# Kernel tuning notes

Measured on AMD Instinct MI355X. Metric: run time of the kernel, lower is better.

Reference implementation:

```python
import jax, jax.numpy as jnp
import numpy as np

D = 2048  # d_model
B = 64    # batch
S = 32    # seq_len (module is designed for 32-step sequences)
C = 8     # number of control embeddings
INITRANGE = 0.1


def setup_inputs() -> dict:
    key = jax.random.key(0)
    ks = jax.random.split(key, 6)

    def lin_w(k):
        return jax.random.uniform(k, (D, D), minval=-INITRANGE, maxval=INITRANGE, dtype=jnp.float32)

    zb = jnp.zeros((D,), dtype=jnp.float32)
    return {
        "sequence": jax.random.normal(ks[0], (B, S, D), dtype=jnp.float32),
        "controls": jax.random.normal(ks[1], (C, B, D), dtype=jnp.float32),
        "Wq": lin_w(ks[2]), "bq": zb,
        "Wk": lin_w(ks[3]), "bk": zb,
        "Wv": lin_w(ks[4]), "bv": zb,
        "Wo": lin_w(ks[5]), "bo": zb,
    }


def reference(sequence, controls, Wq, bq, Wk, bk, Wv, bv, Wo, bo):
    # sequence: (B, S, D); controls: (C, B, D) = stacked list of control embeddings.
    d = sequence.shape[-1]
    queries = sequence @ Wq.T + bq            # (B, S, D)
    keys = controls @ Wk.T + bk               # (C, B, D)  == control_key(c).unsqueeze(1)
    values = controls @ Wv.T + bv             # (C, B, D)
    # bmm(queries, keys^T) with a single key per control -> scores (C, B, S, 1)
    scores = jnp.einsum('bsd,cbd->cbs', queries, keys)[..., None] / jnp.sqrt(jnp.asarray(d, sequence.dtype))
    attn = jax.nn.softmax(scores, axis=-1)    # softmax over a size-1 axis -> exactly 1.0
    attended = attn * values[:, :, None, :]   # (C, B, S, D); bmm(attn, values)
    # dropout is identity in eval mode
    projected = jnp.einsum('cbsd,ed->cbse', attended, Wo) + bo  # per-control output_proj
    # residual accumulation over the control loop == sum over C
    return sequence + projected.sum(axis=0)
```

## Files before the change

kernel.cpp:

```cpp
#include <hip/hip_runtime.h>
#include <hip/hip_bf16.h>

#define DM 2048
#define BB 64
#define SS 32
#define CC 8

typedef __attribute__((ext_vector_type(8))) short short8;
typedef __attribute__((ext_vector_type(4))) short short4v;
typedef __attribute__((ext_vector_type(4))) float f32x4;

static __device__ __forceinline__ short f2bf(float f) {
  union { __hip_bfloat16 h; short s; } u;
  u.h = __float2bfloat16(f);
  return u.s;
}

__global__ void k1_sum_bf16(const float* __restrict__ controls,
                            short* __restrict__ u16) {
  const int idx = blockIdx.x * 128 + threadIdx.x;
  const int b = idx >> 9;
  const int k = (idx & 511) * 4;
  float4 s = make_float4(0.f, 0.f, 0.f, 0.f);
#pragma unroll
  for (int c = 0; c < CC; ++c) {
    const float4 v = *reinterpret_cast<const float4*>(
        controls + ((size_t)c * BB + b) * DM + k);
    s.x += v.x; s.y += v.y; s.z += v.z; s.w += v.w;
  }
  short4v o = {f2bf(s.x), f2bf(s.y), f2bf(s.z), f2bf(s.w)};
  *reinterpret_cast<short4v*>(u16 + (size_t)b * DM + k) = o;
}

__global__ __launch_bounds__(256, 2) void gemm_v16(
    const short* __restrict__ abf, const float* __restrict__ w,
    const float* __restrict__ bias, short* __restrict__ vout) {
  __shared__ float lwW[4][2][16 * 128];
  __shared__ f32x4 red[3][64];

  const int t    = threadIdx.x;
  const int lane = t & 63;
  const int wv   = t >> 6;
  const int e0   = (blockIdx.x & 127) * 16;
  const int b0   = (blockIdx.x >> 7) * 16;
  const int kq   = wv * 512;

  const int wrl = lane >> 5, wg = lane & 31;
  const int r = lane & 15, ksub = lane >> 4;
  const int q = r & 7;

  const short* abase = abf + (size_t)(b0 + r) * DM + kq + ksub * 8;
  short8 areg[2][4];
  f32x4 acc = {0.f, 0.f, 0.f, 0.f};

#define ISSUE_W(c, bsel)                                                      \
  {                                                                           \
    const int ck = kq + (c) * 128;                                            \
    float* wd = &lwW[wv][bsel][0];                                            \
    _Pragma("unroll") for (int i = 0; i < 8; ++i) {                           \
      const int row = 2 * i + wrl;                                            \
      const float* src =                                                      \
          w + (size_t)(e0 + row) * DM + ck + ((wg ^ (row & 7)) << 2);         \
      __builtin_amdgcn_global_load_lds(                                       \
          (const __attribute__((address_space(1))) void*)src,                 \
          (__attribute__((address_space(3))) void*)(wd + i * 256), 16, 0, 0); \
    }                                                                         \
  }
#define LOAD_A(c, bsel)                                                       \
  {                                                                           \
    _Pragma("unroll") for (int s = 0; s < 4; ++s) areg[bsel][s] =             \
        *reinterpret_cast<const short8*>(abase + (c) * 128 + s * 32);         \
  }

  ISSUE_W(0, 0)
  LOAD_A(0, 0)

#pragma unroll
  for (int c = 0; c < 4; ++c) {
    if (c < 3) {
      ISSUE_W(c + 1, (c + 1) & 1)
      LOAD_A(c + 1, (c + 1) & 1)
      asm volatile("s_waitcnt vmcnt(12)" ::: "memory");
    } else {
      asm volatile("s_waitcnt vmcnt(0)" ::: "memory");
    }
    __builtin_amdgcn_sched_barrier(0);

    const float* wb = &lwW[wv][c & 1][0];
#pragma unroll
    for (int s = 0; s < 4; ++s) {
      const int gl = s * 8 + ksub * 2;
      const float4 lo =
          *reinterpret_cast<const float4*>(wb + r * 128 + ((gl ^ q) << 2));
      const float4 hi = *reinterpret_cast<const float4*>(
          wb + r * 128 + (((gl + 1) ^ q) << 2));
      short8 bf;
      bf[0] = f2bf(lo.x); bf[1] = f2bf(lo.y);
      bf[2] = f2bf(lo.z); bf[3] = f2bf(lo.w);
      bf[4] = f2bf(hi.x); bf[5] = f2bf(hi.y);
      bf[6] = f2bf(hi.z); bf[7] = f2bf(hi.w);
      acc = __builtin_amdgcn_mfma_f32_16x16x32_bf16(areg[c & 1][s], bf, acc,
                                                    0, 0, 0);
    }
  }
#undef ISSUE_W
#undef LOAD_A

  if (wv != 0) red[wv - 1][lane] = acc;
  __syncthreads();
  if (wv == 0) {
#pragma unroll
    for (int i = 0; i < 3; ++i) acc += red[i][lane];
    const float be = 8.f * bias[e0 + r];
#pragma unroll
    for (int j = 0; j < 4; ++j)
      vout[(size_t)(b0 + ksub * 4 + j) * DM + e0 + r] = f2bf(acc[j] + be);
  }
}

__global__ __launch_bounds__(512, 2) void gemm_out(
    const short* __restrict__ abf, const float* __restrict__ w,
    const float* __restrict__ bias, const float* __restrict__ seq,
    float* __restrict__ out) {
  __shared__ float lwW[8][2][16 * 64];
  __shared__ f32x4 red[2][3][64];
  __shared__ float ptt[16][32];

  const int t    = threadIdx.x;
  const int lane = t & 63;
  const int wv   = t >> 6;
  const int eh   = wv & 1;
  const int kqi  = wv >> 1;
  const int e0   = (blockIdx.x & 63) * 32;
  const int b0   = (blockIdx.x >> 6) * 16;
  const int ew   = e0 + eh * 16;
  const int kq   = kqi * 512;

  const int rl4 = lane >> 4, g = lane & 15;
  const int r = lane & 15, ksub = lane >> 4;

  const short* abase = abf + (size_t)(b0 + r) * DM + kq + ksub * 8;
  short8 areg[2][2];
  f32x4 acc = {0.f, 0.f, 0.f, 0.f};

  const int bl = t >> 5, rem = t & 31;
  const int ef4 = (rem & 7) * 4, sl = rem >> 3;
  float4 sreg[8];

#define ISSUE_W2(c, bsel)                                                     \
  {                                                                           \
    const int ck = kq + (c) * 64;                                             \
    float* wd = &lwW[wv][bsel][0];                                            \
    _Pragma("unroll") for (int i = 0; i < 4; ++i) {                           \
      const int row = 4 * i + rl4;                                            \
      const float* src =                                                      \
          w + (size_t)(ew + row) * DM + ck + ((g ^ row) << 2);                \
      __builtin_amdgcn_global_load_lds(                                       \
          (const __attribute__((address_space(1))) void*)src,                 \
          (__attribute__((address_space(3))) void*)(wd + i * 256), 16, 0, 0); \
    }                                                                         \
  }
#define LOAD_A2(c, bsel)                                                      \
  {                                                                           \
    areg[bsel][0] = *reinterpret_cast<const short8*>(abase + (c) * 64);       \
    areg[bsel][1] = *reinterpret_cast<const short8*>(abase + (c) * 64 + 32);  \
  }

  ISSUE_W2(0, 0)
  LOAD_A2(0, 0)

#pragma unroll
  for (int c = 0; c < 8; ++c) {
    if (c < 7) {
      ISSUE_W2(c + 1, (c + 1) & 1)
      LOAD_A2(c + 1, (c + 1) & 1)
      asm volatile("s_waitcnt vmcnt(6)" ::: "memory");
    } else {
#pragma unroll
      for (int i = 0; i < 8; ++i) {
        const size_t off =
            ((size_t)(b0 + bl) * SS + (sl + 4 * i)) * DM + e0 + ef4;
        sreg[i] = *reinterpret_cast<const float4*>(seq + off);
      }
      asm volatile("s_waitcnt vmcnt(8)" ::: "memory");
    }
    __builtin_amdgcn_sched_barrier(0);

    const float* wb = &lwW[wv][c & 1][0];
#pragma unroll
    for (int s = 0; s < 2; ++s) {
      const int gl = s * 8 + ksub * 2;
      const float4 lo =
          *reinterpret_cast<const float4*>(wb + r * 64 + ((gl ^ r) << 2));
      const float4 hi = *reinterpret_cast<const float4*>(
          wb + r * 64 + (((gl + 1) ^ r) << 2));
      short8 bf;
      bf[0] = f2bf(lo.x); bf[1] = f2bf(lo.y);
      bf[2] = f2bf(lo.z); bf[3] = f2bf(lo.w);
      bf[4] = f2bf(hi.x); bf[5] = f2bf(hi.y);
      bf[6] = f2bf(hi.z); bf[7] = f2bf(hi.w);
      acc = __builtin_amdgcn_mfma_f32_16x16x32_bf16(areg[c & 1][s], bf, acc,
                                                    0, 0, 0);
    }
  }
#undef ISSUE_W2
#undef LOAD_A2

  if (kqi != 0) red[eh][kqi - 1][lane] = acc;
  __syncthreads();
  if (kqi == 0) {
#pragma unroll
    for (int i = 0; i < 3; ++i) acc += red[eh][i][lane];
    const float be = 8.f * bias[ew + r];
#pragma unroll
    for (int j = 0; j < 4; ++j) ptt[ksub * 4 + j][eh * 16 + r] = acc[j] + be;
  }
  __syncthreads();

  const float4 pv = *reinterpret_cast<const float4*>(&ptt[bl][ef4]);
  asm volatile("s_waitcnt vmcnt(0)" ::: "memory");
#pragma unroll
  for (int i = 0; i < 8; ++i) {
    const size_t off = ((size_t)(b0 + bl) * SS + (sl + 4 * i)) * DM + e0 + ef4;
    *reinterpret_cast<float4*>(out + off) =
        make_float4(sreg[i].x + pv.x, sreg[i].y + pv.y, sreg[i].z + pv.z,
                    sreg[i].w + pv.w);
  }
}

extern "C" void kernel_launch(void* const* d_in, const int* in_sizes, int n_in,
                              void* d_out, int out_size, void* d_ws,
                              size_t ws_size, hipStream_t stream) {
  const float* seq      = (const float*)d_in[0];
  const float* controls = (const float*)d_in[1];
  const float* Wv = (const float*)d_in[6];
  const float* bv = (const float*)d_in[7];
  const float* Wo = (const float*)d_in[8];
  const float* bo = (const float*)d_in[9];
  float* out = (float*)d_out;

  char* ws = (char*)d_ws;
  short* u16 = (short*)(ws);
  short* v16 = (short*)(ws + (512ull << 10));

  k1_sum_bf16<<<256, 128, 0, stream>>>(controls, u16);
  gemm_v16<<<512, 256, 0, stream>>>(u16, Wv, bv, v16);
  gemm_out<<<256, 512, 0, stream>>>(v16, Wo, bo, seq, out);
}
```

Before: 30.49 us.

## Fuse control-sum kernel into first GEMM via grid-wide atomic barrier

Folds the control-embedding sum/bf16 conversion into the first GEMM kernel. Each block computes a slice of the summed controls, then all blocks wait on a global atomic counter before starting the GEMM. This removes one kernel launch but adds a memset launch and a spin barrier that assumes all 512 blocks are co-resident. Separately, the output GEMM now interleaves the sequence residual loads across the k-loop instead of issuing them all at the end.

```diff
diff --git a/kernel.cpp b/kernel.cpp
--- a/kernel.cpp
+++ b/kernel.cpp
@@ -5,6 +5,7 @@
 #define BB 64
 #define SS 32
 #define CC 8
+#define NBA 512
 
 typedef __attribute__((ext_vector_type(8))) short short8;
 typedef __attribute__((ext_vector_type(4))) short short4v;
@@ -16,40 +17,52 @@
   return u.s;
 }
 
-__global__ void k1_sum_bf16(const float* __restrict__ controls,
-                            short* __restrict__ u16) {
-  const int idx = blockIdx.x * 128 + threadIdx.x;
-  const int b = idx >> 9;
-  const int k = (idx & 511) * 4;
-  float4 s = make_float4(0.f, 0.f, 0.f, 0.f);
-#pragma unroll
-  for (int c = 0; c < CC; ++c) {
-    const float4 v = *reinterpret_cast<const float4*>(
-        controls + ((size_t)c * BB + b) * DM + k);
-    s.x += v.x; s.y += v.y; s.z += v.z; s.w += v.w;
-  }
-  short4v o = {f2bf(s.x), f2bf(s.y), f2bf(s.z), f2bf(s.w)};
-  *reinterpret_cast<short4v*>(u16 + (size_t)b * DM + k) = o;
-}
-
-__global__ __launch_bounds__(256, 2) void gemm_v16(
-    const short* __restrict__ abf, const float* __restrict__ w,
-    const float* __restrict__ bias, short* __restrict__ vout) {
+__global__ __launch_bounds__(256, 2) void fused_u_gemm1(
+    const float* __restrict__ controls, const float* __restrict__ w,
+    const float* __restrict__ bias, short* __restrict__ u16,
+    short* __restrict__ vout, int* __restrict__ bar) {
   __shared__ float lwW[4][2][16 * 128];
   __shared__ f32x4 red[3][64];
 
-  const int t    = threadIdx.x;
+  const int t   = threadIdx.x;
+  const int bid = blockIdx.x;
+
+  if (t < 64) {
+    const int idx = bid * 64 + t;
+    const int b = idx >> 9;
+    const int k = (idx & 511) * 4;
+    float4 s = make_float4(0.f, 0.f, 0.f, 0.f);
+#pragma unroll
+    for (int c = 0; c < CC; ++c) {
+      const float4 v = *reinterpret_cast<const float4*>(
+          controls + ((size_t)c * BB + b) * DM + k);
+      s.x += v.x; s.y += v.y; s.z += v.z; s.w += v.w;
+    }
+    short4v o = {f2bf(s.x), f2bf(s.y), f2bf(s.z), f2bf(s.w)};
+    *reinterpret_cast<short4v*>(u16 + (size_t)b * DM + k) = o;
+  }
+
+  __syncthreads();
+  if (t == 0) {
+    __hip_atomic_fetch_add(bar, 1, __ATOMIC_RELEASE, __HIP_MEMORY_SCOPE_AGENT);
+    while (__hip_atomic_fetch_add(bar, 0, __ATOMIC_RELAXED,
+                                  __HIP_MEMORY_SCOPE_AGENT) < NBA)
+      __builtin_amdgcn_s_sleep(10);
+    (void)__hip_atomic_load(bar, __ATOMIC_ACQUIRE, __HIP_MEMORY_SCOPE_AGENT);
+  }
+  __syncthreads();
+
   const int lane = t & 63;
   const int wv   = t >> 6;
-  const int e0   = (blockIdx.x & 127) * 16;
-  const int b0   = (blockIdx.x >> 7) * 16;
+  const int e0   = (bid & 127) * 16;
+  const int b0   = (bid >> 7) * 16;
   const int kq   = wv * 512;
 
   const int wrl = lane >> 5, wg = lane & 31;
   const int r = lane & 15, ksub = lane >> 4;
   const int q = r & 7;
 
-  const short* abase = abf + (size_t)(b0 + r) * DM + kq + ksub * 8;
+  const short* abase = u16 + (size_t)(b0 + r) * DM + kq + ksub * 8;
   short8 areg[2][4];
   f32x4 acc = {0.f, 0.f, 0.f, 0.f};
 
@@ -165,24 +178,26 @@
     areg[bsel][0] = *reinterpret_cast<const short8*>(abase + (c) * 64);       \
     areg[bsel][1] = *reinterpret_cast<const short8*>(abase + (c) * 64 + 32);  \
   }
+#define LOAD_SEQ(i)                                                           \
+  {                                                                           \
+    const size_t off =                                                        \
+        ((size_t)(b0 + bl) * SS + (sl + 4 * (i))) * DM + e0 + ef4;            \
+    sreg[i] = *reinterpret_cast<const float4*>(seq + off);                    \
+  }
 
   ISSUE_W2(0, 0)
   LOAD_A2(0, 0)
+  LOAD_SEQ(0)
 
 #pragma unroll
   for (int c = 0; c < 8; ++c) {
     if (c < 7) {
       ISSUE_W2(c + 1, (c + 1) & 1)
       LOAD_A2(c + 1, (c + 1) & 1)
-      asm volatile("s_waitcnt vmcnt(6)" ::: "memory");
+      LOAD_SEQ(c + 1)
+      asm volatile("s_waitcnt vmcnt(8)" ::: "memory");
     } else {
-#pragma unroll
-      for (int i = 0; i < 8; ++i) {
-        const size_t off =
-            ((size_t)(b0 + bl) * SS + (sl + 4 * i)) * DM + e0 + ef4;
-        sreg[i] = *reinterpret_cast<const float4*>(seq + off);
-      }
-      asm volatile("s_waitcnt vmcnt(8)" ::: "memory");
+      asm volatile("s_waitcnt vmcnt(1)" ::: "memory");
     }
     __builtin_amdgcn_sched_barrier(0);
 
@@ -205,6 +220,7 @@
   }
 #undef ISSUE_W2
 #undef LOAD_A2
+#undef LOAD_SEQ
 
   if (kqi != 0) red[eh][kqi - 1][lane] = acc;
   __syncthreads();
@@ -240,10 +256,11 @@
   float* out = (float*)d_out;
 
   char* ws = (char*)d_ws;
-  short* u16 = (short*)(ws);
+  int*   bar = (int*)(ws);
+  short* u16 = (short*)(ws + (4ull << 10));
   short* v16 = (short*)(ws + (512ull << 10));
 
-  k1_sum_bf16<<<256, 128, 0, stream>>>(controls, u16);
-  gemm_v16<<<512, 256, 0, stream>>>(u16, Wv, bv, v16);
+  hipMemsetAsync(bar, 0, 4096, stream);
+  fused_u_gemm1<<<NBA, 256, 0, stream>>>(controls, Wv, bv, u16, v16, bar);
   gemm_out<<<256, 512, 0, stream>>>(v16, Wo, bo, seq, out);
 }
```

Result: slower. 57.76 us (+89.4%).
